# Performance work log

Measured on AMD Instinct MI355X. Metric: run time of the kernel, lower is better.

Reference implementation:

```python
import jax, jax.numpy as jnp
import numpy as np

B, S, D, H = 2, 2048, 1024, 16
HD = D // H


def setup_inputs() -> dict:
    key = jax.random.key(0)
    ks = jax.random.split(key, 7)
    mk = lambda k, shape, scale=1.0: (jax.random.normal(k, shape, dtype=jnp.float32) * scale)
    w_scale = 1.0 / np.sqrt(D)  # ~nn.Linear init scale
    return {
        "query": mk(ks[0], (B, S, D)),
        "key": mk(ks[1], (B, S, D)),
        "value": mk(ks[2], (B, S, D)),
        "Wq": mk(ks[3], (D, D), w_scale),
        "Wk": mk(ks[4], (D, D), w_scale),
        "Wv": mk(ks[5], (D, D), w_scale),
        "Wo": mk(ks[6], (D, D), w_scale),
    }


def reference(query, key, value, Wq, Wk, Wv, Wo):
    # torch nn.Linear(bias=False): y = x @ W.T, W is (out, in)
    def proj(x, W):
        y = jnp.einsum('bsd,ed->bse', x, W)          # [B, S, D]
        return y.reshape(x.shape[0], x.shape[1], H, HD).transpose(0, 2, 1, 3)  # [B, H, S, HD]

    Q = proj(query, Wq)
    K = proj(key, Wk)
    V = proj(value, Wv)

    # NOTE: original scales by sqrt(embedding_size), not sqrt(head_dim)
    scale = 1.0 / jnp.sqrt(jnp.asarray(D, dtype=Q.dtype))
    scores = jnp.einsum('bhqd,bhkd->bhqk', Q, K) * scale   # [B, H, Q, K]
    attn = jax.nn.softmax(scores, axis=-1)
    ctx = jnp.einsum('bhqk,bhkd->bhqd', attn, V)           # [B, H, Q, HD]
    ctx = ctx.transpose(0, 2, 1, 3).reshape(query.shape[0], query.shape[1], D)
    return jnp.einsum('bsd,ed->bse', ctx, Wo)
```

## Files before the change

kernel.cpp:

```cpp
#include <hip/hip_runtime.h>
#include <hip/hip_bf16.h>


typedef __bf16 bf16x8 __attribute__((ext_vector_type(8)));
typedef float f32x4 __attribute__((ext_vector_type(4)));
typedef float f32x16 __attribute__((ext_vector_type(16)));
typedef int i32x4 __attribute__((ext_vector_type(4)));

static constexpr int Bb = 2, Ss = 2048, Dd = 1024, Hh = 16, HDd = 64;
static constexpr int Mtot = Bb * Ss;

__global__ __launch_bounds__(256) void cast_f32_bf16(const float* __restrict__ src,
                                                     __hip_bfloat16* __restrict__ dst, int n8) {
  int i = blockIdx.x * 256 + threadIdx.x;
  if (i >= n8) return;
  const float4* s4 = (const float4*)src + (size_t)i * 2;
  float4 a = s4[0], b = s4[1];
  union { __hip_bfloat16 h[8]; int4 v; } u;
  u.h[0] = __float2bfloat16(a.x); u.h[1] = __float2bfloat16(a.y);
  u.h[2] = __float2bfloat16(a.z); u.h[3] = __float2bfloat16(a.w);
  u.h[4] = __float2bfloat16(b.x); u.h[5] = __float2bfloat16(b.y);
  u.h[6] = __float2bfloat16(b.z); u.h[7] = __float2bfloat16(b.w);
  ((int4*)dst)[i] = u.v;
}

#define BM 128
#define BN 128
#define BK 64

__device__ __forceinline__ void gload_lds16(const void* g, void* l) {
  __builtin_amdgcn_global_load_lds((const __attribute__((address_space(1))) unsigned*)g,
                                   (__attribute__((address_space(3))) unsigned*)l, 16, 0, 0);
}

__device__ __forceinline__ void storeC(float* C, size_t idx, float v) { C[idx] = v; }
__device__ __forceinline__ void storeC(__hip_bfloat16* C, size_t idx, float v) {
  C[idx] = __float2bfloat16(v);
}

template <typename OutT>
__device__ __forceinline__ void gemm_bt_body(const __hip_bfloat16* __restrict__ A,
                                             const __hip_bfloat16* __restrict__ Bw,
                                             OutT* __restrict__ C, int K, int N) {
  __shared__ __hip_bfloat16 As[BM * BK];
  __shared__ __hip_bfloat16 Bs[BN * BK];
  const int tid = threadIdx.x;
  const int lane = tid & 63;
  const int wid = tid >> 6;
  const int wm = (wid >> 1) * 64;
  const int wn = (wid & 1) * 64;
  const int bm = blockIdx.x, bn = blockIdx.y;
  const int l15 = lane & 15;
  const int lhi = lane >> 4;

  f32x4 zero = {0.f, 0.f, 0.f, 0.f};
  f32x4 acc[4][4];
#pragma unroll
  for (int i = 0; i < 4; ++i)
#pragma unroll
    for (int j = 0; j < 4; ++j) acc[i][j] = zero;

  const size_t abase = (size_t)(bm * BM) * K;
  const size_t bbase = (size_t)(bn * BN) * K;

  for (int k0 = 0; k0 < K; k0 += BK) {
#pragma unroll
    for (int p = 0; p < 4; ++p) {
      int c = p * 256 + tid;
      int row = c >> 3;
      int col = (c & 7) * 8;
      gload_lds16(A + abase + (size_t)row * K + k0 + col, (char*)As + c * 16);
    }
#pragma unroll
    for (int p = 0; p < 4; ++p) {
      int c = p * 256 + tid;
      int row = c >> 3;
      int col = (c & 7) * 8;
      gload_lds16(Bw + bbase + (size_t)row * K + k0 + col, (char*)Bs + c * 16);
    }
    __syncthreads();
#pragma unroll
    for (int kk = 0; kk < 2; ++kk) {
      bf16x8 af[4], bfr[4];
#pragma unroll
      for (int mt = 0; mt < 4; ++mt)
        af[mt] = *(const bf16x8*)&As[(wm + mt * 16 + l15) * BK + kk * 32 + lhi * 8];
#pragma unroll
      for (int nt = 0; nt < 4; ++nt)
        bfr[nt] = *(const bf16x8*)&Bs[(wn + nt * 16 + l15) * BK + kk * 32 + lhi * 8];
#pragma unroll
      for (int mt = 0; mt < 4; ++mt)
#pragma unroll
        for (int nt = 0; nt < 4; ++nt)
          acc[mt][nt] = __builtin_amdgcn_mfma_f32_16x16x32_bf16(af[mt], bfr[nt], acc[mt][nt], 0, 0, 0);
    }
    __syncthreads();
  }

#pragma unroll
  for (int mt = 0; mt < 4; ++mt)
#pragma unroll
    for (int r = 0; r < 4; ++r) {
      int row = bm * BM + wm + mt * 16 + lhi * 4 + r;
#pragma unroll
      for (int nt = 0; nt < 4; ++nt) {
        int col = bn * BN + wn + nt * 16 + l15;
        storeC(C, (size_t)row * N + col, acc[mt][nt][r]);
      }
    }
}

__global__ __launch_bounds__(256) void qkv_proj(
    const __hip_bfloat16* __restrict__ xq, const __hip_bfloat16* __restrict__ xk,
    const __hip_bfloat16* __restrict__ xv, const __hip_bfloat16* __restrict__ wq,
    const __hip_bfloat16* __restrict__ wk, const __hip_bfloat16* __restrict__ wv,
    __hip_bfloat16* __restrict__ Qp, __hip_bfloat16* __restrict__ Kp,
    __hip_bfloat16* __restrict__ Vp) {
  const __hip_bfloat16* A;
  const __hip_bfloat16* W;
  __hip_bfloat16* C;
  if (blockIdx.z == 0) { A = xq; W = wq; C = Qp; }
  else if (blockIdx.z == 1) { A = xk; W = wk; C = Kp; }
  else { A = xv; W = wv; C = Vp; }
  gemm_bt_body<__hip_bfloat16>(A, W, C, Dd, Dd);
}

__global__ __launch_bounds__(256) void out_proj(const __hip_bfloat16* __restrict__ ctx,
                                                const __hip_bfloat16* __restrict__ wo,
                                                float* __restrict__ out) {
  gemm_bt_body<float>(ctx, wo, out, Dd, Dd);
}

__global__ __launch_bounds__(256) void transpose_v(const __hip_bfloat16* __restrict__ Vp,
                                                   __hip_bfloat16* __restrict__ Vt) {
  __shared__ __hip_bfloat16 T[64][72];
  const int tid = threadIdx.x;
  const int s0 = blockIdx.x * 64;
  const int bh = blockIdx.y;
  const int b = bh >> 4, h = bh & 15;
  const __hip_bfloat16* src = Vp + (size_t)b * Ss * Dd + (size_t)h * HDd;
#pragma unroll
  for (int p = 0; p < 2; ++p) {
    int id = p * 256 + tid;
    int r = id >> 3, c8 = (id & 7) * 8;
    *(int4*)&T[r][c8] = *(const int4*)(src + (size_t)(s0 + r) * Dd + c8);
  }
  __syncthreads();
#pragma unroll
  for (int p = 0; p < 2; ++p) {
    int id = p * 256 + tid;
    int d = id >> 3, s8 = (id & 7) * 8;
    union { int4 v; __hip_bfloat16 hh[8]; } u;
#pragma unroll
    for (int j = 0; j < 8; ++j) u.hh[j] = T[s8 + j][d];
    *(int4*)(Vt + ((size_t)bh * HDd + d) * Ss + s0 + s8) = u.v;
  }
}

__global__ __launch_bounds__(256) void attn_kernel(const __hip_bfloat16* __restrict__ Qp,
                                                   const __hip_bfloat16* __restrict__ Kp,
                                                   const __hip_bfloat16* __restrict__ Vt,
                                                   __hip_bfloat16* __restrict__ ctx) {
  constexpr int NT = Ss / 64;
  __shared__ __hip_bfloat16 Ks[2][64 * 64];
  __shared__ __hip_bfloat16 Vs[2][64 * 64];

  const int tid = threadIdx.x;
  const int lane = tid & 63, wid = tid >> 6;
  const int l31 = lane & 31;
  const bool hih = (lane >= 32);
  const int lhi2 = hih ? 1 : 0;
  const int qblk = blockIdx.x, bh = blockIdx.y;
  const int b = bh >> 4, h = bh & 15;
  const size_t head_off = (size_t)b * Ss * Dd + (size_t)h * HDd;
  const size_t vt_off = (size_t)bh * HDd * Ss;
  const int qrow = qblk * 128 + wid * 32 + l31;
  constexpr float scale = 0.03125f;
  constexpr float L2E = 1.44269504f;
  const float la = scale * L2E;

  bf16x8 qf[4];
#pragma unroll
  for (int ksd = 0; ksd < 4; ++ksd)
    qf[ksd] = *(const bf16x8*)(Qp + head_off + (size_t)qrow * Dd + ksd * 16 + lhi2 * 8);

  float m_run = -1e30f, l_run = 0.f;
  f32x16 o[2];
#pragma unroll
  for (int db = 0; db < 2; ++db)
#pragma unroll
    for (int r = 0; r < 16; ++r) o[db][r] = 0.f;

  auto stage = [&](int buf, int kv0) {
#pragma unroll
    for (int p = 0; p < 2; ++p) {
      int c = p * 256 + tid;
      int row = c >> 3;
      int sch = (c & 7) ^ (row & 7);
      gload_lds16(Kp + head_off + (size_t)(kv0 + row) * Dd + sch * 8,
                  (char*)&Ks[buf][0] + c * 16);
      gload_lds16(Vt + vt_off + (size_t)row * Ss + kv0 + sch * 8,
                  (char*)&Vs[buf][0] + c * 16);
    }
  };

  stage(0, 0);
  __syncthreads();
  int cur = 0;

  for (int t = 0; t < NT; ++t) {
    if (t + 1 < NT) stage(cur ^ 1, (t + 1) * 64);

    f32x16 st[2];
#pragma unroll
    for (int kb = 0; kb < 2; ++kb)
#pragma unroll
      for (int r = 0; r < 16; ++r) st[kb][r] = 0.f;
    const char* kbase = (const char*)&Ks[cur][0];
#pragma unroll
    for (int kb = 0; kb < 2; ++kb) {
      int row = kb * 32 + l31;
#pragma unroll
      for (int ksd = 0; ksd < 4; ++ksd) {
        bf16x8 kfrag = *(const bf16x8*)(kbase + row * 128 +
                                        (((ksd * 2 + lhi2) ^ (row & 7)) << 4));
        st[kb] = __builtin_amdgcn_mfma_f32_32x32x16_bf16(kfrag, qf[ksd], st[kb], 0, 0, 0);
      }
    }

    float tm = st[0][0];
#pragma unroll
    for (int r = 1; r < 16; ++r) tm = fmaxf(tm, st[0][r]);
#pragma unroll
    for (int r = 0; r < 16; ++r) tm = fmaxf(tm, st[1][r]);
    tm *= scale;
    tm = fmaxf(tm, __shfl_xor(tm, 32));

    float mn = fmaxf(m_run, tm);
    float fcorr = __expf(m_run - mn);
    m_run = mn;
    const float lb = -mn * L2E;

#pragma unroll
    for (int kb = 0; kb < 2; ++kb)
#pragma unroll
      for (int r = 0; r < 16; ++r) st[kb][r] = exp2f(fmaf(st[kb][r], la, lb));

    float ps = 0.f;
#pragma unroll
    for (int kb = 0; kb < 2; ++kb)
#pragma unroll
      for (int r = 0; r < 16; ++r) ps += st[kb][r];
    ps += __shfl_xor(ps, 32);
    l_run = l_run * fcorr + ps;

#pragma unroll
    for (int db = 0; db < 2; ++db)
#pragma unroll
      for (int r = 0; r < 16; ++r) o[db][r] *= fcorr;

    int cpk[2][4][2];
#pragma unroll
    for (int kb = 0; kb < 2; ++kb)
#pragma unroll
      for (int g = 0; g < 4; ++g)
#pragma unroll
        for (int i = 0; i < 2; ++i) {
          int rr;
          float lo = st[kb][g * 4 + 2 * i], hi = st[kb][g * 4 + 2 * i + 1];
          asm("v_cvt_pk_bf16_f32 %0, %1, %2" : "=v"(rr) : "v"(lo), "v"(hi));
          cpk[kb][g][i] = rr;
        }

    int own[2][2][2], rcv[2][2][2];
#pragma unroll
    for (int kb = 0; kb < 2; ++kb)
#pragma unroll
      for (int m = 0; m < 2; ++m)
#pragma unroll
        for (int i = 0; i < 2; ++i) {
          int cA = cpk[kb][2 * m][i];
          int cB = cpk[kb][2 * m + 1][i];
          int pay = hih ? cA : cB;
          own[kb][m][i] = hih ? cB : cA;
          rcv[kb][m][i] = __shfl_xor(pay, 32);
        }

    const char* vbase = (const char*)&Vs[cur][0];
#pragma unroll
    for (int ks = 0; ks < 4; ++ks) {
      const int kb = ks >> 1, m = ks & 1;
      int w0 = hih ? rcv[kb][m][0] : own[kb][m][0];
      int w1 = hih ? rcv[kb][m][1] : own[kb][m][1];
      int w2 = hih ? own[kb][m][0] : rcv[kb][m][0];
      int w3 = hih ? own[kb][m][1] : rcv[kb][m][1];
      i32x4 bw = {w0, w1, w2, w3};
      bf16x8 pfrag = __builtin_bit_cast(bf16x8, bw);
#pragma unroll
      for (int db = 0; db < 2; ++db) {
        int row = db * 32 + l31;
        bf16x8 vfrag = *(const bf16x8*)(vbase + row * 128 +
                                        (((ks * 2 + lhi2) ^ (row & 7)) << 4));
        o[db] = __builtin_amdgcn_mfma_f32_32x32x16_bf16(vfrag, pfrag, o[db], 0, 0, 0);
      }
    }

    __syncthreads();
    cur ^= 1;
  }

  float inv = 1.f / l_run;
  __hip_bfloat16* crow = ctx + head_off + (size_t)qrow * Dd;
#pragma unroll
  for (int db = 0; db < 2; ++db)
#pragma unroll
    for (int g = 0; g < 4; ++g) {
      union { uint2 v; __hip_bfloat16 hh[4]; } u;
#pragma unroll
      for (int a = 0; a < 4; ++a) u.hh[a] = __float2bfloat16(o[db][g * 4 + a] * inv);
      *(uint2*)(crow + db * 32 + 8 * g + 4 * lhi2) = u.v;
    }
}

extern "C" void kernel_launch(void* const* d_in, const int* in_sizes, int n_in,
                              void* d_out, int out_size, void* d_ws, size_t ws_size,
                              hipStream_t stream) {
  const float* q_f = (const float*)d_in[0];
  const float* k_f = (const float*)d_in[1];
  const float* v_f = (const float*)d_in[2];
  const float* wq_f = (const float*)d_in[3];
  const float* wk_f = (const float*)d_in[4];
  const float* wv_f = (const float*)d_in[5];
  const float* wo_f = (const float*)d_in[6];
  float* out = (float*)d_out;

  const size_t act = (size_t)Mtot * Dd;
  const size_t wsz = (size_t)Dd * Dd;
  char* ws = (char*)d_ws;
  __hip_bfloat16* qb = (__hip_bfloat16*)ws;   ws += act * 2;
  __hip_bfloat16* kb = (__hip_bfloat16*)ws;   ws += act * 2;
  __hip_bfloat16* vb = (__hip_bfloat16*)ws;   ws += act * 2;
  __hip_bfloat16* wqb = (__hip_bfloat16*)ws;  ws += wsz * 2;
  __hip_bfloat16* wkb = (__hip_bfloat16*)ws;  ws += wsz * 2;
  __hip_bfloat16* wvb = (__hip_bfloat16*)ws;  ws += wsz * 2;
  __hip_bfloat16* wob = (__hip_bfloat16*)ws;  ws += wsz * 2;
  __hip_bfloat16* Qp = (__hip_bfloat16*)ws;   ws += act * 2;
  __hip_bfloat16* Kp = (__hip_bfloat16*)ws;   ws += act * 2;
  __hip_bfloat16* Vp = (__hip_bfloat16*)ws;   ws += act * 2;
  __hip_bfloat16* Vt = (__hip_bfloat16*)ws;   ws += act * 2;
  __hip_bfloat16* ctxb = (__hip_bfloat16*)ws; ws += act * 2;

  cast_f32_bf16<<<(int)(act / 8 / 256), 256, 0, stream>>>(q_f, qb, (int)(act / 8));
  cast_f32_bf16<<<(int)(act / 8 / 256), 256, 0, stream>>>(k_f, kb, (int)(act / 8));
  cast_f32_bf16<<<(int)(act / 8 / 256), 256, 0, stream>>>(v_f, vb, (int)(act / 8));
  cast_f32_bf16<<<(int)(wsz / 8 / 256), 256, 0, stream>>>(wq_f, wqb, (int)(wsz / 8));
  cast_f32_bf16<<<(int)(wsz / 8 / 256), 256, 0, stream>>>(wk_f, wkb, (int)(wsz / 8));
  cast_f32_bf16<<<(int)(wsz / 8 / 256), 256, 0, stream>>>(wv_f, wvb, (int)(wsz / 8));
  cast_f32_bf16<<<(int)(wsz / 8 / 256), 256, 0, stream>>>(wo_f, wob, (int)(wsz / 8));

  dim3 gq(Mtot / BM, Dd / BN, 3);
  qkv_proj<<<gq, 256, 0, stream>>>(qb, kb, vb, wqb, wkb, wvb, Qp, Kp, Vp);

  dim3 gt(Ss / 64, Bb * Hh);
  transpose_v<<<gt, 256, 0, stream>>>(Vp, Vt);

  dim3 ga(Ss / 128, Bb * Hh);
  attn_kernel<<<ga, 256, 0, stream>>>(Qp, Kp, Vt, ctxb);

  dim3 go(Mtot / BM, Dd / BN);
  out_proj<<<go, 256, 0, stream>>>(ctxb, wob, out);
}
```

Before: 186.8 us.

## Split attention KV range across two wave groups, fuse casts, lazy rescale

The seven cast launches are merged into a single 2D-grid kernel. The attention kernel now uses 512 threads: two groups of four waves each handle half of the KV sequence for the same query block, and their partial softmax states are merged through LDS at the end. Block IDs are remapped for locality, and the running max is only updated when it grows by more than a threshold, which skips the per-tile rescale of the output. The max and sum reductions are vectorized. This trades more LDS and a final merge step for more waves in flight and less softmax work per tile.

```diff
diff --git a/kernel.cpp b/kernel.cpp
--- a/kernel.cpp
+++ b/kernel.cpp
@@ -3,15 +3,34 @@
 
 
 typedef __bf16 bf16x8 __attribute__((ext_vector_type(8)));
+typedef float f32x2 __attribute__((ext_vector_type(2)));
 typedef float f32x4 __attribute__((ext_vector_type(4)));
+typedef float f32x8 __attribute__((ext_vector_type(8)));
 typedef float f32x16 __attribute__((ext_vector_type(16)));
 typedef int i32x4 __attribute__((ext_vector_type(4)));
 
 static constexpr int Bb = 2, Ss = 2048, Dd = 1024, Hh = 16, HDd = 64;
 static constexpr int Mtot = Bb * Ss;
 
-__global__ __launch_bounds__(256) void cast_f32_bf16(const float* __restrict__ src,
-                                                     __hip_bfloat16* __restrict__ dst, int n8) {
+__global__ __launch_bounds__(256) void cast_all(
+    const float* __restrict__ a0, const float* __restrict__ a1, const float* __restrict__ a2,
+    const float* __restrict__ a3, const float* __restrict__ a4, const float* __restrict__ a5,
+    const float* __restrict__ a6, __hip_bfloat16* __restrict__ d0, __hip_bfloat16* __restrict__ d1,
+    __hip_bfloat16* __restrict__ d2, __hip_bfloat16* __restrict__ d3,
+    __hip_bfloat16* __restrict__ d4, __hip_bfloat16* __restrict__ d5,
+    __hip_bfloat16* __restrict__ d6, int nact8, int nw8) {
+  const float* src;
+  __hip_bfloat16* dst;
+  int n8;
+  switch (blockIdx.y) {
+    case 0: src = a0; dst = d0; n8 = nact8; break;
+    case 1: src = a1; dst = d1; n8 = nact8; break;
+    case 2: src = a2; dst = d2; n8 = nact8; break;
+    case 3: src = a3; dst = d3; n8 = nw8; break;
+    case 4: src = a4; dst = d4; n8 = nw8; break;
+    case 5: src = a5; dst = d5; n8 = nw8; break;
+    default: src = a6; dst = d6; n8 = nw8; break;
+  }
   int i = blockIdx.x * 256 + threadIdx.x;
   if (i >= n8) return;
   const float4* s4 = (const float4*)src + (size_t)i * 2;
@@ -157,24 +176,32 @@
   }
 }
 
-__global__ __launch_bounds__(256) void attn_kernel(const __hip_bfloat16* __restrict__ Qp,
+__global__ __launch_bounds__(512) void attn_kernel(const __hip_bfloat16* __restrict__ Qp,
                                                    const __hip_bfloat16* __restrict__ Kp,
                                                    const __hip_bfloat16* __restrict__ Vt,
                                                    __hip_bfloat16* __restrict__ ctx) {
   constexpr int NT = Ss / 64;
-  __shared__ __hip_bfloat16 Ks[2][64 * 64];
-  __shared__ __hip_bfloat16 Vs[2][64 * 64];
+  constexpr int HT = NT / 2;
+  __shared__ __align__(16) __hip_bfloat16 Ks[2][2][64 * 64];
+  __shared__ __align__(16) __hip_bfloat16 Vs[2][2][64 * 64];
 
   const int tid = threadIdx.x;
   const int lane = tid & 63, wid = tid >> 6;
+  const int grp = wid >> 2;
+  const int qw = wid & 3;
   const int l31 = lane & 31;
   const bool hih = (lane >= 32);
   const int lhi2 = hih ? 1 : 0;
-  const int qblk = blockIdx.x, bh = blockIdx.y;
+
+  const int bid = blockIdx.x;
+  const int w = (bid & 7) * 64 + (bid >> 3);
+  const int qblk = w & 15;
+  const int bh = w >> 4;
+
   const int b = bh >> 4, h = bh & 15;
   const size_t head_off = (size_t)b * Ss * Dd + (size_t)h * HDd;
   const size_t vt_off = (size_t)bh * HDd * Ss;
-  const int qrow = qblk * 128 + wid * 32 + l31;
+  const int qrow = qblk * 128 + qw * 32 + l31;
   constexpr float scale = 0.03125f;
   constexpr float L2E = 1.44269504f;
   const float la = scale * L2E;
@@ -191,32 +218,34 @@
 #pragma unroll
     for (int r = 0; r < 16; ++r) o[db][r] = 0.f;
 
+  const int gtid = tid & 255;
   auto stage = [&](int buf, int kv0) {
 #pragma unroll
     for (int p = 0; p < 2; ++p) {
-      int c = p * 256 + tid;
+      int c = p * 256 + gtid;
       int row = c >> 3;
       int sch = (c & 7) ^ (row & 7);
       gload_lds16(Kp + head_off + (size_t)(kv0 + row) * Dd + sch * 8,
-                  (char*)&Ks[buf][0] + c * 16);
+                  (char*)&Ks[grp][buf][0] + c * 16);
       gload_lds16(Vt + vt_off + (size_t)row * Ss + kv0 + sch * 8,
-                  (char*)&Vs[buf][0] + c * 16);
+                  (char*)&Vs[grp][buf][0] + c * 16);
     }
   };
 
-  stage(0, 0);
+  const int t0 = grp * HT;
+  stage(0, t0 * 64);
   __syncthreads();
   int cur = 0;
 
-  for (int t = 0; t < NT; ++t) {
-    if (t + 1 < NT) stage(cur ^ 1, (t + 1) * 64);
+  for (int tt = 0; tt < HT; ++tt) {
+    if (tt + 1 < HT) stage(cur ^ 1, (t0 + tt + 1) * 64);
 
     f32x16 st[2];
 #pragma unroll
     for (int kb = 0; kb < 2; ++kb)
 #pragma unroll
       for (int r = 0; r < 16; ++r) st[kb][r] = 0.f;
-    const char* kbase = (const char*)&Ks[cur][0];
+    const char* kbase = (const char*)&Ks[grp][cur][0];
 #pragma unroll
     for (int kb = 0; kb < 2; ++kb) {
       int row = kb * 32 + l31;
@@ -228,36 +257,43 @@
       }
     }
 
-    float tm = st[0][0];
-#pragma unroll
-    for (int r = 1; r < 16; ++r) tm = fmaxf(tm, st[0][r]);
-#pragma unroll
-    for (int r = 0; r < 16; ++r) tm = fmaxf(tm, st[1][r]);
-    tm *= scale;
+    f32x16 mm16 = __builtin_elementwise_max(st[0], st[1]);
+    f32x8 mm8 = __builtin_elementwise_max(
+        __builtin_shufflevector(mm16, mm16, 0, 1, 2, 3, 4, 5, 6, 7),
+        __builtin_shufflevector(mm16, mm16, 8, 9, 10, 11, 12, 13, 14, 15));
+    f32x4 mm4 = __builtin_elementwise_max(__builtin_shufflevector(mm8, mm8, 0, 1, 2, 3),
+                                          __builtin_shufflevector(mm8, mm8, 4, 5, 6, 7));
+    f32x2 mm2 = __builtin_elementwise_max(__builtin_shufflevector(mm4, mm4, 0, 1),
+                                          __builtin_shufflevector(mm4, mm4, 2, 3));
+    float tm = fmaxf(mm2[0], mm2[1]) * scale;
     tm = fmaxf(tm, __shfl_xor(tm, 32));
 
-    float mn = fmaxf(m_run, tm);
-    float fcorr = __expf(m_run - mn);
-    m_run = mn;
-    const float lb = -mn * L2E;
-
-#pragma unroll
-    for (int kb = 0; kb < 2; ++kb)
-#pragma unroll
-      for (int r = 0; r < 16; ++r) st[kb][r] = exp2f(fmaf(st[kb][r], la, lb));
-
-    float ps = 0.f;
-#pragma unroll
-    for (int kb = 0; kb < 2; ++kb)
-#pragma unroll
-      for (int r = 0; r < 16; ++r) ps += st[kb][r];
+    if (!__all(tm - m_run <= 8.f)) {
+      float mn = fmaxf(m_run, tm);
+      float fc = __expf(m_run - mn);
+      m_run = mn;
+      l_run *= fc;
+      o[0] *= fc;
+      o[1] *= fc;
+    }
+    const float lb = -m_run * L2E;
+
+#pragma unroll
+    for (int kb = 0; kb < 2; ++kb) {
+      st[kb] = st[kb] * la + lb;
+#pragma unroll
+      for (int r = 0; r < 16; ++r) st[kb][r] = exp2f(st[kb][r]);
+    }
+
+    f32x16 s16 = st[0] + st[1];
+    f32x8 s8 = __builtin_shufflevector(s16, s16, 0, 1, 2, 3, 4, 5, 6, 7) +
+               __builtin_shufflevector(s16, s16, 8, 9, 10, 11, 12, 13, 14, 15);
+    f32x4 s4 = __builtin_shufflevector(s8, s8, 0, 1, 2, 3) +
+               __builtin_shufflevector(s8, s8, 4, 5, 6, 7);
+    f32x2 s2 = __builtin_shufflevector(s4, s4, 0, 1) + __builtin_shufflevector(s4, s4, 2, 3);
+    float ps = s2[0] + s2[1];
     ps += __shfl_xor(ps, 32);
-    l_run = l_run * fcorr + ps;
-
-#pragma unroll
-    for (int db = 0; db < 2; ++db)
-#pragma unroll
-      for (int r = 0; r < 16; ++r) o[db][r] *= fcorr;
+    l_run += ps;
 
     int cpk[2][4][2];
 #pragma unroll
@@ -286,7 +322,7 @@
           rcv[kb][m][i] = __shfl_xor(pay, 32);
         }
 
-    const char* vbase = (const char*)&Vs[cur][0];
+    const char* vbase = (const char*)&Vs[grp][cur][0];
 #pragma unroll
     for (int ks = 0; ks < 4; ++ks) {
       const int kb = ks >> 1, m = ks & 1;
@@ -309,17 +345,39 @@
     cur ^= 1;
   }
 
-  float inv = 1.f / l_run;
-  __hip_bfloat16* crow = ctx + head_off + (size_t)qrow * Dd;
-#pragma unroll
-  for (int db = 0; db < 2; ++db)
-#pragma unroll
-    for (int g = 0; g < 4; ++g) {
-      union { uint2 v; __hip_bfloat16 hh[4]; } u;
-#pragma unroll
-      for (int a = 0; a < 4; ++a) u.hh[a] = __float2bfloat16(o[db][g * 4 + a] * inv);
-      *(uint2*)(crow + db * 32 + 8 * g + 4 * lhi2) = u.v;
-    }
+  float* mbuf = (float*)&Ks[0][0][0];
+  if (grp == 1) {
+    float* slot = mbuf + ((qw * 64 + lane) * 36);
+    *(f32x16*)(slot) = o[0];
+    *(f32x16*)(slot + 16) = o[1];
+    slot[32] = m_run;
+    slot[33] = l_run;
+  }
+  __syncthreads();
+  if (grp == 0) {
+    float* slot = mbuf + ((qw * 64 + lane) * 36);
+    f32x16 o2a = *(f32x16*)(slot);
+    f32x16 o2b = *(f32x16*)(slot + 16);
+    float m2 = slot[32], l2 = slot[33];
+    float mn = fmaxf(m_run, m2);
+    float f1 = __expf(m_run - mn), f2 = __expf(m2 - mn);
+    float l = l_run * f1 + l2 * f2;
+    float inv = 1.f / l;
+    float c1 = f1 * inv, c2 = f2 * inv;
+    o[0] = o[0] * c1 + o2a * c2;
+    o[1] = o[1] * c1 + o2b * c2;
+
+    __hip_bfloat16* crow = ctx + head_off + (size_t)qrow * Dd;
+#pragma unroll
+    for (int db = 0; db < 2; ++db)
+#pragma unroll
+      for (int g = 0; g < 4; ++g) {
+        union { uint2 v; __hip_bfloat16 hh[4]; } u;
+#pragma unroll
+        for (int a = 0; a < 4; ++a) u.hh[a] = __float2bfloat16(o[db][g * 4 + a]);
+        *(uint2*)(crow + db * 32 + 8 * g + 4 * lhi2) = u.v;
+      }
+  }
 }
 
 extern "C" void kernel_launch(void* const* d_in, const int* in_sizes, int n_in,
@@ -350,13 +408,9 @@
   __hip_bfloat16* Vt = (__hip_bfloat16*)ws;   ws += act * 2;
   __hip_bfloat16* ctxb = (__hip_bfloat16*)ws; ws += act * 2;
 
-  cast_f32_bf16<<<(int)(act / 8 / 256), 256, 0, stream>>>(q_f, qb, (int)(act / 8));
-  cast_f32_bf16<<<(int)(act / 8 / 256), 256, 0, stream>>>(k_f, kb, (int)(act / 8));
-  cast_f32_bf16<<<(int)(act / 8 / 256), 256, 0, stream>>>(v_f, vb, (int)(act / 8));
-  cast_f32_bf16<<<(int)(wsz / 8 / 256), 256, 0, stream>>>(wq_f, wqb, (int)(wsz / 8));
-  cast_f32_bf16<<<(int)(wsz / 8 / 256), 256, 0, stream>>>(wk_f, wkb, (int)(wsz / 8));
-  cast_f32_bf16<<<(int)(wsz / 8 / 256), 256, 0, stream>>>(wv_f, wvb, (int)(wsz / 8));
-  cast_f32_bf16<<<(int)(wsz / 8 / 256), 256, 0, stream>>>(wo_f, wob, (int)(wsz / 8));
+  dim3 gc((unsigned)(act / 8 / 256), 7);
+  cast_all<<<gc, 256, 0, stream>>>(q_f, k_f, v_f, wq_f, wk_f, wv_f, wo_f, qb, kb, vb, wqb,
+                                   wkb, wvb, wob, (int)(act / 8), (int)(wsz / 8));
 
   dim3 gq(Mtot / BM, Dd / BN, 3);
   qkv_proj<<<gq, 256, 0, stream>>>(qb, kb, vb, wqb, wkb, wvb, Qp, Kp, Vp);
@@ -364,8 +418,7 @@
   dim3 gt(Ss / 64, Bb * Hh);
   transpose_v<<<gt, 256, 0, stream>>>(Vp, Vt);
 
-  dim3 ga(Ss / 128, Bb * Hh);
-  attn_kernel<<<ga, 256, 0, stream>>>(Qp, Kp, Vt, ctxb);
+  attn_kernel<<<(Ss / 128) * (Bb * Hh), 512, 0, stream>>>(Qp, Kp, Vt, ctxb);
 
   dim3 go(Mtot / BM, Dd / BN);
   out_proj<<<go, 256, 0, stream>>>(ctxb, wob, out);
```

New measurement: 179.9 us. -3.7%, faster.
